# Optimization experiments

Hardware: AMD Instinct MI355X
Metric: run time of the kernel (lower is better)

The kernel has to match this reference:

```python
import jax, jax.numpy as jnp
import numpy as np

N = 50_000          # num nodes
E = 800_000         # num edges
D = 32              # input/hidden dim
NUM_LAYERS = 6
BOUNDARY_FILL = 100.0


def setup_inputs() -> dict:
    key = jax.random.key(0)
    ks = jax.random.split(key, 10)
    return {
        "node_in": jax.random.randint(ks[0], (E,), 0, N, dtype=jnp.int32),
        "node_out": jax.random.randint(ks[1], (E,), 0, N, dtype=jnp.int32),
        "edge_weight": jax.random.uniform(ks[2], (E,), dtype=jnp.float32),
        "h_index": 0,
        "query_weight": jax.random.normal(ks[3], (1, D), dtype=jnp.float32) * 0.1,
        "rel_W": jax.random.normal(ks[4], (NUM_LAYERS, D, D), dtype=jnp.float32) / np.sqrt(D),
        "rel_b": jnp.zeros((NUM_LAYERS, D), dtype=jnp.float32),
        "lin_W": jax.random.normal(ks[5], (NUM_LAYERS, 13 * D, D), dtype=jnp.float32) / np.sqrt(13 * D),
        "lin_b": jnp.zeros((NUM_LAYERS, D), dtype=jnp.float32),
        "mlp_W1": jax.random.normal(ks[6], (2 * D, 2 * D), dtype=jnp.float32) / np.sqrt(2 * D),
        "mlp_b1": jnp.zeros((2 * D,), dtype=jnp.float32),
        "mlp_W2": jax.random.normal(ks[7], (2 * D, 1), dtype=jnp.float32) / np.sqrt(2 * D),
        "mlp_b2": jnp.zeros((1,), dtype=jnp.float32),
    }


def reference(node_in, node_out, edge_weight, h_index, query_weight,
              rel_W, rel_b, lin_W, lin_b, mlp_W1, mlp_b1, mlp_W2, mlp_b2):
    # query = self.query(r_index) with r_index = 0, batch = 1
    query = query_weight[:1]                                # [1, D]
    boundary = jnp.full((N, 1, D), BOUNDARY_FILL, dtype=jnp.float32)
    boundary = boundary.at[h_index, 0].set(0.0)             # boundary[h][0] = 0

    loop = jnp.arange(N, dtype=node_out.dtype)
    node_in_aug = jnp.concatenate([node_in, loop])          # boundary rows act as self-loop msgs
    node_out_aug = jnp.concatenate([node_out, loop])
    ew_aug = jnp.concatenate([edge_weight, jnp.ones((N,), edge_weight.dtype)])

    degree_out = jax.ops.segment_sum(edge_weight, node_out, num_segments=N) + 1.0  # [N]
    count = jax.ops.segment_sum(jnp.ones_like(ew_aug), node_out_aug, num_segments=N)  # [N]

    # PNA degree scalers (identity / amplification / attenuation)
    scale = jnp.log(degree_out)
    scale = scale / jnp.mean(scale)
    scales = jnp.stack([jnp.ones_like(scale), scale, 1.0 / jnp.clip(scale, 1e-2)], axis=-1)  # [N,3]

    w = ew_aug[:, None, None]
    cnt = count[:, None, None]

    layer_input = boundary
    predecessor = jnp.zeros((N,), dtype=node_in.dtype)
    for i in range(NUM_LAYERS):
        # dependent relation embedding: relation_linear(query), relation id 0 everywhere
        rel_input = query @ rel_W[i] + rel_b[i]             # [1, D]
        message = layer_input[node_in] * rel_input[None]    # [E,1,D] distmult
        msg_aug = jnp.concatenate([message, boundary], axis=0)  # [E+N,1,D]
        wm = msg_aug * w

        mean = jax.ops.segment_sum(wm, node_out_aug, num_segments=N) / cnt
        sq_mean = jax.ops.segment_sum(jnp.square(msg_aug) * w, node_out_aug, num_segments=N) / cnt
        mx = jax.ops.segment_max(wm, node_out_aug, num_segments=N)
        mn = jax.ops.segment_min(wm, node_out_aug, num_segments=N)
        std = jnp.sqrt(jnp.clip(sq_mean - jnp.square(mean), 1e-6))

        feats = jnp.stack([mean, mx, mn, std], axis=-1).reshape(N, 1, 4 * D)
        update = (feats[..., None] * scales[:, None, None, :]).reshape(N, 1, 12 * D)
        hidden = jax.nn.relu(
            jnp.concatenate([layer_input, update], axis=-1) @ lin_W[i] + lin_b[i]
        )  # [N,1,D]

        if i == NUM_LAYERS - 1:
            # predecessor: source node of the strongest incoming (weighted) message
            msg_score = wm.sum(axis=(1, 2))                 # [E+N]
            seg_max = jax.ops.segment_max(msg_score, node_out_aug, num_segments=N)
            cand = jnp.where(msg_score >= seg_max[node_out_aug], node_in_aug,
                             jnp.asarray(N, node_in_aug.dtype))
            predecessor = jax.ops.segment_min(cand, node_out_aug, num_segments=N)
        layer_input = hidden

    node_query = jnp.broadcast_to(query[None], (N, 1, D))
    output = jnp.concatenate([layer_input, node_query], axis=-1)  # [N,1,2D]
    feature = jnp.transpose(output, (1, 0, 2))                    # [1,N,2D]
    h = jax.nn.relu(feature @ mlp_W1 + mlp_b1)
    score = (h @ mlp_W2 + mlp_b2).squeeze(-1)                     # [1,N]
    return score, predecessor
```

## Files before the change

### kernel.cpp

```cpp
#include <hip/hip_runtime.h>
#include <math.h>

#define NN 50000
#define EE 800000
#define DD 32
#define BSTR 64
#define NPART 8
#define CPB 128

typedef float v2f __attribute__((ext_vector_type(2)));


__global__ __launch_bounds__(256) void k_zero(float* p, int count){
  int i = blockIdx.x*256 + threadIdx.x;
  if (i < count) p[i] = 0.f;
}

__global__ __launch_bounds__(256) void k_fillcsr(const int* __restrict__ node_in,
                                                 const int* __restrict__ node_out,
                                                 const float* __restrict__ ew,
                                                 int* __restrict__ cursor,
                                                 int2* __restrict__ csr){
  int part  = blockIdx.x & (NPART-1);
  int group = blockIdx.x >> 3;
  const int per = (EE + CPB - 1) / CPB;
  int e0 = group * per;
  int e1 = (e0 + per < EE) ? (e0 + per) : EE;
  unsigned lo = (unsigned)part * 6250u;
  unsigned hi = lo + 6250u;
  for (int e = e0 + threadIdx.x; e < e1; e += 256){
    unsigned o = (unsigned)node_out[e];
    if (o >= lo && o < hi){
      int pos = atomicAdd(&cursor[o], 1);
      int2 v; v.x = node_in[e]; v.y = __float_as_int(ew[e]);
      csr[o*BSTR + pos] = v;
    }
  }
}

__global__ __launch_bounds__(256) void k_sumw(int2* __restrict__ csr,
                                              const int* __restrict__ cursor,
                                              float* __restrict__ deg_w,
                                              float* __restrict__ logsum){
  __shared__ float sf[256];
  int t = threadIdx.x; int n = blockIdx.x*256 + t;
  float s = 0.f;
  if (n < NN){
    int deg = cursor[n];
    int2* row = csr + n*BSTR;
    for (int i = 0; i < deg; ++i) s += __int_as_float(row[i].y);
    deg_w[n] = s;
    #pragma unroll
    for (int i = 0; i < 8; ++i) row[deg + i] = make_int2(0, 0);
  }
  sf[t] = (n < NN) ? logf(s + 1.f) : 0.f;
  __syncthreads();
  for (int off = 128; off > 0; off >>= 1){
    if (t < off) sf[t] += sf[t+off];
    __syncthreads();
  }
  if (t == 0) atomicAdd(logsum, sf[0]);
}

__global__ __launch_bounds__(256) void k_prep(const float* __restrict__ qw,
                                              const float* __restrict__ rel_W,
                                              const float* __restrict__ rel_b,
                                              const float* __restrict__ W1,
                                              const float* __restrict__ b1,
                                              float* __restrict__ rel6,
                                              float* __restrict__ qc){
  int t = threadIdx.x;
  if (t < 192){
    int l = t >> 5, j = t & 31;
    float s = rel_b[t];
    for (int d = 0; d < 32; ++d) s += qw[d] * rel_W[l*1024 + d*32 + j];
    rel6[t] = s;
  } else if (t < 256){
    int j = t - 192;
    float s = b1[j];
    for (int k = 0; k < 32; ++k) s += qw[k] * W1[(32+k)*64 + j];
    qc[j] = s;
  }
}

__global__ __launch_bounds__(256) void k_init_h(const int* __restrict__ hidx,
                                                float* __restrict__ h){
  int i = blockIdx.x*256 + threadIdx.x;
  int hv = *hidx;
  if (i < NN*DD) h[i] = ((i >> 5) == hv) ? 0.f : 100.f;
}

__global__ __launch_bounds__(256) void k_dot(const float* __restrict__ h,
                                             const float* __restrict__ rel6,
                                             float* __restrict__ tdot){
  int n0 = blockIdx.x*256 + threadIdx.x;
  int n = (n0 < NN) ? n0 : NN-1;
  const float* relr = rel6 + 5*32;
  float s = 0.f;
  #pragma unroll
  for (int d = 0; d < 32; ++d) s += h[n*32 + d] * relr[d];
  if (n0 < NN) tdot[n0] = s;
}

template<bool PRED>
__global__ __launch_bounds__(512, 6) void k_layer(const float* __restrict__ h,
                                               const float* __restrict__ rel6,
                                               const int* __restrict__ cursor,
                                               const int2* __restrict__ csr,
                                               const int* __restrict__ hidx,
                                               const float* __restrict__ tdot,
                                               const float* __restrict__ lin_W,
                                               const float* __restrict__ lin_b,
                                               const float* __restrict__ deg_w,
                                               const float* __restrict__ logsum,
                                               float* __restrict__ h_next,
                                               float* __restrict__ pred_out,
                                               int l){
  __shared__ float sh[128*65];
  int tid = threadIdx.x;
  int base = blockIdx.x * 64;
  int hv0 = *hidx;

  {
    int nl   = tid >> 3;
    int quad = tid & 7;
    float4 r4 = ((const float4*)(rel6 + l*32))[quad];
    int n0 = base + nl;
    bool valid = n0 < NN;
    int n = valid ? n0 : NN-1;
    int deg = cursor[n];
    int s0 = n*BSTR, s1 = s0 + deg;
    float S10=0.f,S11=0.f,S12=0.f,S13=0.f;
    float S20=0.f,S21=0.f,S22=0.f,S23=0.f;
    float M0=-INFINITY,M1=-INFINITY,M2=-INFINITY,M3=-INFINITY;
    float m0=INFINITY,m1=INFINITY,m2=INFINITY,m3=INFINITY;
    float best=-INFINITY; int bi=NN;

#define ACC1(C, A, T) { \
    float w = __int_as_float(C.y); \
    float p0=w*A.x, p1=w*A.y, p2=w*A.z, p3=w*A.w; \
    S10+=p0; S11+=p1; S12+=p2; S13+=p3; \
    S20+=p0*A.x; S21+=p1*A.y; S22+=p2*A.z; S23+=p3*A.w; \
    M0=fmaxf(M0,p0); M1=fmaxf(M1,p1); M2=fmaxf(M2,p2); M3=fmaxf(M3,p3); \
    m0=fminf(m0,p0); m1=fminf(m1,p1); m2=fminf(m2,p2); m3=fminf(m3,p3); \
    if (PRED){ \
      float sv = w*T; \
      if (sv > best){ best = sv; bi = C.x; } \
      else if (sv == best && C.x < bi) bi = C.x; \
    } }

    int2 cA = csr[s0],   cB = csr[s0+1], cC = csr[s0+2], cD = csr[s0+3];
    int e = s0;
    for (; e + 4 <= s1; e += 4){
      float4 a  = ((const float4*)(h + cA.x*32))[quad];
      float4 b  = ((const float4*)(h + cB.x*32))[quad];
      float4 c4 = ((const float4*)(h + cC.x*32))[quad];
      float4 d4 = ((const float4*)(h + cD.x*32))[quad];
      float tA=0.f, tB=0.f, tC=0.f, tD=0.f;
      if (PRED){ tA = tdot[cA.x]; tB = tdot[cB.x]; tC = tdot[cC.x]; tD = tdot[cD.x]; }
      int2 nA = csr[e+4], nB = csr[e+5], nC = csr[e+6], nD = csr[e+7];
      ACC1(cA, a, tA)
      ACC1(cB, b, tB)
      ACC1(cC, c4, tC)
      ACC1(cD, d4, tD)
      cA = nA; cB = nB; cC = nC; cD = nD;
    }
    if (e < s1){
      float4 a = ((const float4*)(h + cA.x*32))[quad];
      float tA = 0.f; if (PRED) tA = tdot[cA.x];
      ACC1(cA, a, tA)
      if (e + 1 < s1){
        float4 b = ((const float4*)(h + cB.x*32))[quad];
        float tB = 0.f; if (PRED) tB = tdot[cB.x];
        ACC1(cB, b, tB)
        if (e + 2 < s1){
          float4 c4 = ((const float4*)(h + cC.x*32))[quad];
          float tC = 0.f; if (PRED) tC = tdot[cC.x];
          ACC1(cC, c4, tC)
        }
      }
    }
#undef ACC1

    float bnd = (n == hv0) ? 0.f : 100.f;
    float cntf = (float)(deg + 1);
#define FIN(cc, rc, S1c, S2c, Mc, mc) { \
    float mxv, mnv; \
    if (deg > 0){ \
      float em = (rc >= 0.f) ? rc*Mc : rc*mc; \
      float en = (rc >= 0.f) ? rc*mc : rc*Mc; \
      mxv = fmaxf(em, bnd); mnv = fminf(en, bnd); \
    } else { mxv = bnd; mnv = bnd; } \
    float meanv = (rc*S1c + bnd) / cntf; \
    float sq    = (rc*rc*S2c + bnd*bnd) / cntf; \
    float sdv   = sqrtf(fmaxf(sq - meanv*meanv, 1e-6f)); \
    int d = quad*4 + cc; \
    sh[(d*4+0)*65 + nl] = meanv; \
    sh[(d*4+1)*65 + nl] = mxv; \
    sh[(d*4+2)*65 + nl] = mnv; \
    sh[(d*4+3)*65 + nl] = sdv; }
    FIN(0, r4.x, S10, S20, M0, m0)
    FIN(1, r4.y, S11, S21, M1, m1)
    FIN(2, r4.z, S12, S22, M2, m2)
    FIN(3, r4.w, S13, S23, M3, m3)
#undef FIN
    if (PRED && valid && quad == 0){
      float ss = (n == hv0) ? 0.f : 3200.f;
      if (ss > best){ best = ss; bi = n; }
      else if (ss == best && n < bi) bi = n;
      pred_out[n] = (float)bi;
    }
  }
  __syncthreads();

  {
    const float* Wl = lin_W + (size_t)l * 13312;
    int lane = tid & 63;
    int j0 = __builtin_amdgcn_readfirstlane((tid >> 6) * 4);
    int n0 = base + lane;
    int n = (n0 < NN) ? n0 : NN-1;
    float mean = *logsum / (float)NN;
    float sc = logf(deg_w[n] + 1.f) / mean;
    float iv = 1.f / fmaxf(sc, 0.01f);
    const float4* hr = (const float4*)(h + (size_t)n*32);
    float4 x0=hr[0],x1=hr[1],x2=hr[2],x3=hr[3],x4=hr[4],x5=hr[5],x6=hr[6],x7=hr[7];
    v2f a01, a23;
    a01[0] = lin_b[l*32 + j0 + 0]; a01[1] = lin_b[l*32 + j0 + 1];
    a23[0] = lin_b[l*32 + j0 + 2]; a23[1] = lin_b[l*32 + j0 + 3];

#define KONE(XV, K) { \
    v2f xv2; xv2[0] = XV; xv2[1] = XV; \
    const v2f* wr2 = (const v2f*)(Wl + (K)*32 + j0); \
    a01 += xv2 * wr2[0]; \
    a23 += xv2 * wr2[1]; }
#define KQ(X, KB) KONE(X.x, KB+0) KONE(X.y, KB+1) KONE(X.z, KB+2) KONE(X.w, KB+3)
    KQ(x0, 0) KQ(x1, 4) KQ(x2, 8) KQ(x3, 12)
    KQ(x4, 16) KQ(x5, 20) KQ(x6, 24) KQ(x7, 28)
#undef KQ
#undef KONE

    for (int kp = 0; kp < 128; ++kp){
      float f = sh[kp*65 + lane];
      int d = kp >> 2, c = kp & 3;
      const v2f* w2 = (const v2f*)(Wl + (32 + d*12 + c*3)*32 + j0);
      float f1 = f*sc, f2 = f*iv;
      v2f fv;  fv[0]=f;  fv[1]=f;
      v2f f1v; f1v[0]=f1; f1v[1]=f1;
      v2f f2v; f2v[0]=f2; f2v[1]=f2;
      a01 += fv*w2[0] + f1v*w2[16] + f2v*w2[32];
      a23 += fv*w2[1] + f1v*w2[17] + f2v*w2[33];
    }

    if (n0 < NN){
      float vs[4] = { a01[0], a01[1], a23[0], a23[1] };
      #pragma unroll
      for (int j = 0; j < 4; ++j)
        h_next[n0*32 + j0 + j] = fmaxf(vs[j], 0.f);
    }
  }
}

__global__ __launch_bounds__(256) void k_mlp(const float* __restrict__ h,
                                             const float* __restrict__ qc,
                                             const float* __restrict__ W1,
                                             const float* __restrict__ W2,
                                             const float* __restrict__ b2,
                                             float* __restrict__ out_score){
  int n0 = blockIdx.x*256 + threadIdx.x;
  int n = (n0 < NN) ? n0 : NN-1;
  float xr[32];
  const float4* hr = (const float4*)(h + (size_t)n*32);
  #pragma unroll
  for (int q = 0; q < 8; ++q){
    float4 x = hr[q];
    xr[q*4+0]=x.x; xr[q*4+1]=x.y; xr[q*4+2]=x.z; xr[q*4+3]=x.w;
  }
  float acc[64];
  #pragma unroll
  for (int j = 0; j < 64; ++j) acc[j] = qc[j];
  #pragma unroll
  for (int k = 0; k < 32; ++k){
    float xv = xr[k];
    const float* wr = W1 + k*64;
    #pragma unroll
    for (int j = 0; j < 64; ++j) acc[j] += xv * wr[j];
  }
  float s = b2[0];
  #pragma unroll
  for (int j = 0; j < 64; ++j) s += fmaxf(acc[j], 0.f) * W2[j];
  if (n0 < NN) out_score[n0] = s;
}

extern "C" void kernel_launch(void* const* d_in, const int* in_sizes, int n_in,
                              void* d_out, int out_size, void* d_ws, size_t ws_size,
                              hipStream_t stream){
  const int*   node_in  = (const int*)d_in[0];
  const int*   node_out = (const int*)d_in[1];
  const float* ew       = (const float*)d_in[2];
  const int*   hidx     = (const int*)d_in[3];
  const float* qw       = (const float*)d_in[4];
  const float* rel_W    = (const float*)d_in[5];
  const float* rel_b    = (const float*)d_in[6];
  const float* lin_W    = (const float*)d_in[7];
  const float* lin_b    = (const float*)d_in[8];
  const float* W1       = (const float*)d_in[9];
  const float* b1       = (const float*)d_in[10];
  const float* W2       = (const float*)d_in[11];
  const float* b2       = (const float*)d_in[12];
  float* out_score = (float*)d_out;
  float* out_pred  = out_score + NN;

  char* w = (char*)d_ws;
  size_t off = 0;
  auto take = [&](size_t bytes)->char*{
    char* p = w + off;
    off = (off + bytes + 255) & ~(size_t)255;
    return p;
  };
  size_t bucket_elems = (size_t)NN * BSTR;
  int2*  csr      = (int2*)take(bucket_elems*8);
  char*  zb       = take((size_t)NN*4 + (size_t)NN*4 + 256);
  int*   cursor   = (int*)zb;
  float* deg_w    = (float*)(cursor + NN);
  float* logsum   = (float*)(deg_w + NN);
  int zc = NN + NN + 64;

  float* rel6      = (float*)take(192*4);
  float* qc        = (float*)take(64*4);
  float* tdot      = (float*)take((size_t)NN*4);
  float* h_a       = (float*)take((size_t)NN*32*4);
  float* h_b       = (float*)take((size_t)NN*32*4);

  int nb  = (NN + 255) / 256;
  int nlb = (NN + 63) / 64;
  k_zero   <<<(zc+255)/256, 256, 0, stream>>>((float*)zb, zc);
  k_fillcsr<<<NPART*CPB, 256, 0, stream>>>(node_in, node_out, ew, cursor, csr);
  k_sumw   <<<nb, 256, 0, stream>>>(csr, cursor, deg_w, logsum);
  k_prep   <<<1, 256, 0, stream>>>(qw, rel_W, rel_b, W1, b1, rel6, qc);
  k_init_h <<<(NN*DD+255)/256, 256, 0, stream>>>(hidx, h_a);

  float* hc = h_a;
  float* hn = h_b;
  for (int l = 0; l < 6; ++l){
    if (l == 5){
      k_dot<<<nb, 256, 0, stream>>>(hc, rel6, tdot);
      k_layer<true><<<nlb, 512, 0, stream>>>(hc, rel6, cursor, csr, hidx, tdot,
                                             lin_W, lin_b, deg_w, logsum,
                                             hn, out_pred, l);
    } else {
      k_layer<false><<<nlb, 512, 0, stream>>>(hc, rel6, cursor, csr, hidx, tdot,
                                              lin_W, lin_b, deg_w, logsum,
                                              hn, out_pred, l);
    }
    float* t1 = hc; hc = hn; hn = t1;
  }
  k_mlp<<<nb, 256, 0, stream>>>(hc, qc, W1, W2, b2, out_score);
}
```

Before: 461.1 us.

## Specialize first layer for constant boundary input and parallelize degree sum

Adds a dedicated first-layer kernel that derives each message from whether its source is the head node, since the initial hidden state is the constant boundary. This removes the boundary initialization kernel and the random gathers of hidden rows in layer 0. The identity part of the linear layer is folded into a precomputed column sum of lin_W. The degree-weight sum kernel now uses 8 lanes per node with shuffle reductions instead of one thread per node, improving coalescing. The cost is extra code duplication for the specialized layer.

Result: no change. 453.4 us (-1.7%).

```diff
diff --git a/kernel.cpp b/kernel.cpp
--- a/kernel.cpp
+++ b/kernel.cpp
@@ -43,17 +43,21 @@
                                               float* __restrict__ deg_w,
                                               float* __restrict__ logsum){
   __shared__ float sf[256];
-  int t = threadIdx.x; int n = blockIdx.x*256 + t;
+  int t = threadIdx.x;
+  int g = t >> 3, lane = t & 7;
+  int n = blockIdx.x*32 + g;
   float s = 0.f;
   if (n < NN){
     int deg = cursor[n];
     int2* row = csr + n*BSTR;
-    for (int i = 0; i < deg; ++i) s += __int_as_float(row[i].y);
-    deg_w[n] = s;
-    #pragma unroll
-    for (int i = 0; i < 8; ++i) row[deg + i] = make_int2(0, 0);
-  }
-  sf[t] = (n < NN) ? logf(s + 1.f) : 0.f;
+    for (int i = lane; i < deg; i += 8) s += __int_as_float(row[i].y);
+    s += __shfl_xor(s, 1);
+    s += __shfl_xor(s, 2);
+    s += __shfl_xor(s, 4);
+    row[deg + lane] = make_int2(0, 0);
+    if (lane == 0) deg_w[n] = s;
+  }
+  sf[t] = (n < NN && lane == 0) ? logf(s + 1.f) : 0.f;
   __syncthreads();
   for (int off = 128; off > 0; off >>= 1){
     if (t < off) sf[t] += sf[t+off];
@@ -62,13 +66,15 @@
   if (t == 0) atomicAdd(logsum, sf[0]);
 }
 
-__global__ __launch_bounds__(256) void k_prep(const float* __restrict__ qw,
+__global__ __launch_bounds__(320) void k_prep(const float* __restrict__ qw,
                                               const float* __restrict__ rel_W,
                                               const float* __restrict__ rel_b,
                                               const float* __restrict__ W1,
                                               const float* __restrict__ b1,
+                                              const float* __restrict__ lin_W,
                                               float* __restrict__ rel6,
-                                              float* __restrict__ qc){
+                                              float* __restrict__ qc,
+                                              float* __restrict__ wcol){
   int t = threadIdx.x;
   if (t < 192){
     int l = t >> 5, j = t & 31;
@@ -80,14 +86,12 @@
     float s = b1[j];
     for (int k = 0; k < 32; ++k) s += qw[k] * W1[(32+k)*64 + j];
     qc[j] = s;
-  }
-}
-
-__global__ __launch_bounds__(256) void k_init_h(const int* __restrict__ hidx,
-                                                float* __restrict__ h){
-  int i = blockIdx.x*256 + threadIdx.x;
-  int hv = *hidx;
-  if (i < NN*DD) h[i] = ((i >> 5) == hv) ? 0.f : 100.f;
+  } else if (t < 288){
+    int j = t - 256;
+    float s = 0.f;
+    for (int k = 0; k < 32; ++k) s += lin_W[k*32 + j];
+    wcol[j] = s;
+  }
 }
 
 __global__ __launch_bounds__(256) void k_dot(const float* __restrict__ h,
@@ -100,6 +104,113 @@
   #pragma unroll
   for (int d = 0; d < 32; ++d) s += h[n*32 + d] * relr[d];
   if (n0 < NN) tdot[n0] = s;
+}
+
+__global__ __launch_bounds__(512, 6) void k_layer0(const float* __restrict__ rel6,
+                                               const int* __restrict__ cursor,
+                                               const int2* __restrict__ csr,
+                                               const int* __restrict__ hidx,
+                                               const float* __restrict__ lin_W,
+                                               const float* __restrict__ lin_b,
+                                               const float* __restrict__ wcol,
+                                               const float* __restrict__ deg_w,
+                                               const float* __restrict__ logsum,
+                                               float* __restrict__ h_next){
+  __shared__ float sh[128*65];
+  int tid = threadIdx.x;
+  int base = blockIdx.x * 64;
+  int hv0 = *hidx;
+
+  {
+    int nl   = tid >> 3;
+    int quad = tid & 7;
+    float4 r4 = ((const float4*)(rel6))[quad];
+    int n0 = base + nl;
+    int n = (n0 < NN) ? n0 : NN-1;
+    int deg = cursor[n];
+    int s0 = n*BSTR, s1 = s0 + deg;
+    float S1=0.f, S2=0.f, M=-INFINITY, m=INFINITY;
+
+#define ACCS(C) { \
+    float w  = __int_as_float(C.y); \
+    float hv = (C.x == hv0) ? 0.f : 100.f; \
+    float wm = w * hv; \
+    S1 += wm; S2 += wm * hv; \
+    M = fmaxf(M, wm); m = fminf(m, wm); }
+
+    int2 cA = csr[s0],   cB = csr[s0+1], cC = csr[s0+2], cD = csr[s0+3];
+    int e = s0;
+    for (; e + 4 <= s1; e += 4){
+      int2 nA = csr[e+4], nB = csr[e+5], nC = csr[e+6], nD = csr[e+7];
+      ACCS(cA) ACCS(cB) ACCS(cC) ACCS(cD)
+      cA = nA; cB = nB; cC = nC; cD = nD;
+    }
+    if (e < s1){
+      ACCS(cA)
+      if (e + 1 < s1){
+        ACCS(cB)
+        if (e + 2 < s1) ACCS(cC)
+      }
+    }
+#undef ACCS
+
+    float bnd = (n == hv0) ? 0.f : 100.f;
+    float cntf = (float)(deg + 1);
+#define FIN(cc, rc) { \
+    float mxv, mnv; \
+    if (deg > 0){ \
+      float em = (rc >= 0.f) ? rc*M : rc*m; \
+      float en = (rc >= 0.f) ? rc*m : rc*M; \
+      mxv = fmaxf(em, bnd); mnv = fminf(en, bnd); \
+    } else { mxv = bnd; mnv = bnd; } \
+    float meanv = (rc*S1 + bnd) / cntf; \
+    float sq    = (rc*rc*S2 + bnd*bnd) / cntf; \
+    float sdv   = sqrtf(fmaxf(sq - meanv*meanv, 1e-6f)); \
+    int d = quad*4 + cc; \
+    sh[(d*4+0)*65 + nl] = meanv; \
+    sh[(d*4+1)*65 + nl] = mxv; \
+    sh[(d*4+2)*65 + nl] = mnv; \
+    sh[(d*4+3)*65 + nl] = sdv; }
+    FIN(0, r4.x) FIN(1, r4.y) FIN(2, r4.z) FIN(3, r4.w)
+#undef FIN
+  }
+  __syncthreads();
+
+  {
+    const float* Wl = lin_W;
+    int lane = tid & 63;
+    int j0 = __builtin_amdgcn_readfirstlane((tid >> 6) * 4);
+    int n0 = base + lane;
+    int n = (n0 < NN) ? n0 : NN-1;
+    float mean = *logsum / (float)NN;
+    float sc = logf(deg_w[n] + 1.f) / mean;
+    float iv = 1.f / fmaxf(sc, 0.01f);
+    float bndn = (n == hv0) ? 0.f : 100.f;
+    v2f a01, a23;
+    a01[0] = lin_b[j0+0] + bndn*wcol[j0+0];
+    a01[1] = lin_b[j0+1] + bndn*wcol[j0+1];
+    a23[0] = lin_b[j0+2] + bndn*wcol[j0+2];
+    a23[1] = lin_b[j0+3] + bndn*wcol[j0+3];
+
+    for (int kp = 0; kp < 128; ++kp){
+      float f = sh[kp*65 + lane];
+      int d = kp >> 2, c = kp & 3;
+      const v2f* w2 = (const v2f*)(Wl + (32 + d*12 + c*3)*32 + j0);
+      float f1 = f*sc, f2 = f*iv;
+      v2f fv;  fv[0]=f;  fv[1]=f;
+      v2f f1v; f1v[0]=f1; f1v[1]=f1;
+      v2f f2v; f2v[0]=f2; f2v[1]=f2;
+      a01 += fv*w2[0] + f1v*w2[16] + f2v*w2[32];
+      a23 += fv*w2[1] + f1v*w2[17] + f2v*w2[33];
+    }
+
+    if (n0 < NN){
+      float vs[4] = { a01[0], a01[1], a23[0], a23[1] };
+      #pragma unroll
+      for (int j = 0; j < 4; ++j)
+        h_next[n0*32 + j0 + j] = fmaxf(vs[j], 0.f);
+    }
+  }
 }
 
 template<bool PRED>
@@ -327,21 +438,25 @@
 
   float* rel6      = (float*)take(192*4);
   float* qc        = (float*)take(64*4);
+  float* wcol      = (float*)take(32*4);
   float* tdot      = (float*)take((size_t)NN*4);
   float* h_a       = (float*)take((size_t)NN*32*4);
   float* h_b       = (float*)take((size_t)NN*32*4);
 
   int nb  = (NN + 255) / 256;
+  int nsb = (NN + 31) / 32;
   int nlb = (NN + 63) / 64;
   k_zero   <<<(zc+255)/256, 256, 0, stream>>>((float*)zb, zc);
   k_fillcsr<<<NPART*CPB, 256, 0, stream>>>(node_in, node_out, ew, cursor, csr);
-  k_sumw   <<<nb, 256, 0, stream>>>(csr, cursor, deg_w, logsum);
-  k_prep   <<<1, 256, 0, stream>>>(qw, rel_W, rel_b, W1, b1, rel6, qc);
-  k_init_h <<<(NN*DD+255)/256, 256, 0, stream>>>(hidx, h_a);
+  k_sumw   <<<nsb, 256, 0, stream>>>(csr, cursor, deg_w, logsum);
+  k_prep   <<<1, 320, 0, stream>>>(qw, rel_W, rel_b, W1, b1, lin_W, rel6, qc, wcol);
+
+  k_layer0<<<nlb, 512, 0, stream>>>(rel6, cursor, csr, hidx, lin_W, lin_b,
+                                    wcol, deg_w, logsum, h_a);
 
   float* hc = h_a;
   float* hn = h_b;
-  for (int l = 0; l < 6; ++l){
+  for (int l = 1; l < 6; ++l){
     if (l == 5){
       k_dot<<<nb, 256, 0, stream>>>(hc, rel6, tdot);
       k_layer<true><<<nlb, 512, 0, stream>>>(hc, rel6, cursor, csr, hidx, tdot,
```
